# Kernel tuning notes

Measured on AMD Instinct MI355X. Metric: run time of the kernel, lower is better.

## Reference

```python
import jax, jax.numpy as jnp
import numpy as np

V = 1000   # vocab_size
E = 1024   # encoder_output_dim
D = 512    # decoder_hidden_dim
A = 512    # attention_hidden_dim
T = 128    # token_embedding_size
B = 128    # batch
P = 196    # num_pix (14x14)
L = 257    # latex length -> 256 decode steps


def setup_inputs() -> dict:
    key = jax.random.key(0)
    ks = jax.random.split(key, 16)
    def p(k, shape, scale=0.05):
        return (jax.random.normal(k, shape, jnp.float32) * scale)
    return dict(
        features=jax.random.normal(ks[0], (B, P, E), jnp.float32),
        latexes=jax.random.randint(ks[1], (B, L), 0, V),
        emb=p(ks[2], (V, T)),
        Wenc=p(ks[3], (A, E)), benc=jnp.zeros((A,), jnp.float32),
        Wdec=p(ks[4], (A, D)), bdec=jnp.zeros((A,), jnp.float32),
        Wattn=p(ks[5], (1, A)), battn=jnp.zeros((1,), jnp.float32),
        W1ih=p(ks[6], (4 * D, E + T)), W1hh=p(ks[7], (4 * D, D)),
        b1ih=jnp.zeros((4 * D,), jnp.float32), b1hh=jnp.zeros((4 * D,), jnp.float32),
        W2ih=p(ks[8], (4 * D, D)), W2hh=p(ks[9], (4 * D, D)),
        b2ih=jnp.zeros((4 * D,), jnp.float32), b2hh=jnp.zeros((4 * D,), jnp.float32),
        Wh0=p(ks[10], (D, E)), bh0=jnp.zeros((D,), jnp.float32),
        Wc0=p(ks[11], (D, E)), bc0=jnp.zeros((D,), jnp.float32),
        Wg=p(ks[12], (E, D)), bg=jnp.zeros((E,), jnp.float32),
        Wf=p(ks[13], (V, D)), bf=jnp.zeros((V,), jnp.float32),
    )


def _lstm_cell(x, h, c, Wih, Whh, bih, bhh):
    # torch.nn.LSTMCell: gates order i, f, g, o
    g = x @ Wih.T + bih + h @ Whh.T + bhh
    i, f, gg, o = jnp.split(g, 4, axis=1)
    c_new = jax.nn.sigmoid(f) * c + jax.nn.sigmoid(i) * jnp.tanh(gg)
    h_new = jax.nn.sigmoid(o) * jnp.tanh(c_new)
    return h_new, c_new


def reference(features, latexes, emb, Wenc, benc, Wdec, bdec, Wattn, battn,
              W1ih, W1hh, b1ih, b1hh, W2ih, W2hh, b2ih, b2hh,
              Wh0, bh0, Wc0, bc0, Wg, bg, Wf, bf):
    seq_length = latexes.shape[1] - 1
    embeds = emb[latexes]                      # [B, L, T]
    mean_enc = features.mean(axis=1)           # [B, E]
    h1 = mean_enc @ Wh0.T + bh0
    c1 = mean_enc @ Wc0.T + bc0
    h2, c2 = h1, c1
    # encoder branch of attention is step-invariant; hoist out of the loop
    enc_t = features @ Wenc.T + benc           # [B, P, A]
    wa = Wattn[0]                              # [A]
    ba = battn[0]

    def step(carry, emb_s):
        h1, c1, h2, c2 = carry
        dec_t = h2 @ Wdec.T + bdec                         # [B, A]
        attn = jnp.tanh(enc_t + dec_t[:, None, :]) @ wa + ba  # [B, P]
        alpha = jax.nn.softmax(attn, axis=1)
        awe = jnp.einsum('bp,bpe->be', alpha, features)    # [B, E]
        x1 = jnp.concatenate([emb_s, awe], axis=1)         # [B, T+E]
        # NOTE: original computes gate = sigmoid(Wg h2 + bg) and multiplies the
        # attention encoding AFTER lstm1_input was built -> dead code; omitted.
        h1n, c1n = _lstm_cell(x1, h1, c1, W1ih, W1hh, b1ih, b1hh)
        h2n, c2n = _lstm_cell(h1n, h2, c2, W2ih, W2hh, b2ih, b2hh)
        out = h2n @ Wf.T + bf                              # [B, V]
        return (h1n, c1n, h2n, c2n), (out, alpha)

    emb_seq = jnp.swapaxes(embeds[:, :seq_length], 0, 1)   # [S, B, T]
    _, (preds, alphas) = jax.lax.scan(step, (h1, c1, h2, c2), emb_seq)
    preds = jnp.swapaxes(preds, 0, 1)                      # [B, S, V]
    alphas = jnp.swapaxes(alphas, 0, 1)                    # [B, S, P]
    return preds, alphas
```

## Files before the change

kernel.cpp:

```cpp
#include <hip/hip_runtime.h>
#include <hip/hip_bf16.h>
#include <stdint.h>

#define VV 1000
#define EE 1024
#define DD 512
#define AA 512
#define TT 128
#define BB 128
#define PP 196
#define SS 256

typedef unsigned short ushort_t;
typedef __attribute__((ext_vector_type(8))) short short8;
typedef __attribute__((ext_vector_type(4))) float floatx4;
typedef __attribute__((ext_vector_type(4))) unsigned short ushort4_t;
typedef __attribute__((ext_vector_type(8))) unsigned short ushort8_t;

__device__ __forceinline__ float bf2f(unsigned short h) {
    return __uint_as_float(((unsigned int)h) << 16);
}
__device__ __forceinline__ unsigned short f2bf(float x) {
    unsigned int u = __float_as_uint(x);
    unsigned int r = (u + 0x7fffu + ((u >> 16) & 1u)) >> 16;
    return (unsigned short)r;
}
__device__ __forceinline__ float sigmoidf_(float x) { return 1.f / (1.f + __expf(-x)); }
__device__ __forceinline__ float tanhf_(float x) {
    float e = __expf(2.f * x);
    return 1.f - 2.f / (e + 1.f);
}


__global__ void cvt_kernel(const float* __restrict__ src, ushort_t* __restrict__ dst, int n) {
    int i = blockIdx.x * 256 + threadIdx.x;
    if (i < n) dst[i] = f2bf(src[i]);
}

__global__ void mean_kernel(const float* __restrict__ feat, float* __restrict__ meanv) {
    int idx = blockIdx.x * 256 + threadIdx.x;
    int b = idx >> 10;
    int e = idx & 1023;
    const float* p = feat + (size_t)b * PP * 1024 + e;
    float s = 0.f;
    for (int pp = 0; pp < PP; ++pp) s += p[(size_t)pp * 1024];
    meanv[idx] = s * (1.f / 196.f);
}

__global__ __launch_bounds__(256) void init_kernel(
    const float* __restrict__ meanv, const float* __restrict__ Wh0, const float* __restrict__ bh0,
    const float* __restrict__ Wc0, const float* __restrict__ bc0,
    float* __restrict__ c1, float* __restrict__ c2,
    ushort_t* __restrict__ h1b, ushort_t* __restrict__ h2b) {
    int b = blockIdx.x, t = threadIdx.x;
    __shared__ float ml[1024];
    for (int i = t; i < 1024; i += 256) ml[i] = meanv[b * 1024 + i];
    __syncthreads();
    for (int d = t; d < 512; d += 256) {
        const float4* wh = (const float4*)(Wh0 + (size_t)d * 1024);
        const float4* wc = (const float4*)(Wc0 + (size_t)d * 1024);
        float ah = bh0[d], ac = bc0[d];
        #pragma unroll 4
        for (int j = 0; j < 256; ++j) {
            float4 w = wh[j];
            ah += w.x * ml[4 * j] + w.y * ml[4 * j + 1] + w.z * ml[4 * j + 2] + w.w * ml[4 * j + 3];
        }
        #pragma unroll 4
        for (int j = 0; j < 256; ++j) {
            float4 w = wc[j];
            ac += w.x * ml[4 * j] + w.y * ml[4 * j + 1] + w.z * ml[4 * j + 2] + w.w * ml[4 * j + 3];
        }
        c1[b * 512 + d] = ac;
        c2[b * 512 + d] = ac;
        ushort_t hb = f2bf(ah);
        h1b[b * 512 + d] = hb;
        h2b[b * 512 + d] = hb;
    }
}

__global__ __launch_bounds__(256) void enc_gemm(
    const ushort_t* __restrict__ feat_bf, const ushort_t* __restrict__ wenc_bf,
    const float* __restrict__ benc, ushort_t* __restrict__ enc_bf) {
    const int t = threadIdx.x, blk = blockIdx.x;
    const int bm = (blk % 392) * 64, bn = (blk / 392) * 64;
    const int lane = t & 63, wv = t >> 6;
    const int n = lane & 15, q = lane >> 4;
    const int arow = bm + wv * 16 + n;
    const short8* ap = (const short8*)(feat_bf + (size_t)arow * 1024 + q * 8);
    const short8* bp0 = (const short8*)(wenc_bf + (size_t)(bn + 0 * 16 + n) * 1024 + q * 8);
    const short8* bp1 = (const short8*)(wenc_bf + (size_t)(bn + 1 * 16 + n) * 1024 + q * 8);
    const short8* bp2 = (const short8*)(wenc_bf + (size_t)(bn + 2 * 16 + n) * 1024 + q * 8);
    const short8* bp3 = (const short8*)(wenc_bf + (size_t)(bn + 3 * 16 + n) * 1024 + q * 8);
    floatx4 acc0 = {0.f, 0.f, 0.f, 0.f}, acc1 = acc0, acc2 = acc0, acc3 = acc0;
    for (int ks = 0; ks < 32; ++ks) {
        short8 a8 = ap[ks * 4];
        acc0 = __builtin_amdgcn_mfma_f32_16x16x32_bf16(a8, bp0[ks * 4], acc0, 0, 0, 0);
        acc1 = __builtin_amdgcn_mfma_f32_16x16x32_bf16(a8, bp1[ks * 4], acc1, 0, 0, 0);
        acc2 = __builtin_amdgcn_mfma_f32_16x16x32_bf16(a8, bp2[ks * 4], acc2, 0, 0, 0);
        acc3 = __builtin_amdgcn_mfma_f32_16x16x32_bf16(a8, bp3[ks * 4], acc3, 0, 0, 0);
    }
    #pragma unroll
    for (int r = 0; r < 4; ++r) {
        int m = bm + wv * 16 + q * 4 + r;
        int a0 = bn + n;
        enc_bf[(size_t)m * 512 + a0] = f2bf(acc0[r] + benc[a0]);
        enc_bf[(size_t)m * 512 + a0 + 16] = f2bf(acc1[r] + benc[a0 + 16]);
        enc_bf[(size_t)m * 512 + a0 + 32] = f2bf(acc2[r] + benc[a0 + 32]);
        enc_bf[(size_t)m * 512 + a0 + 48] = f2bf(acc3[r] + benc[a0 + 48]);
    }
}


__global__ __launch_bounds__(256) void step_attn_preds(
    const ushort_t* __restrict__ enc_bf, const ushort_t* __restrict__ feat_bf,
    const ushort_t* __restrict__ wdec_bf, const ushort_t* __restrict__ wf_bf,
    const ushort_t* __restrict__ emb_bf, ushort_t* __restrict__ x1_bf,
    const ushort_t* __restrict__ h2cur, const int* __restrict__ latexes,
    const float* __restrict__ wattn, const float* __restrict__ battn,
    const float* __restrict__ bdec, const float* __restrict__ bfv,
    float* __restrict__ out, int s) {
    const int t = threadIdx.x;
    const int blk = blockIdx.x;
    if (blk < BB) {
        if (s >= SS) return;
        const int b = blk;
        __shared__ float dec_lds[512];
        __shared__ float wa_lds[512];
        __shared__ float h2row[512];
        __shared__ float red[256];
        __shared__ float attn_lds[256];
        __shared__ float alpha_lds[200];
        for (int i = t; i < 512; i += 256) {
            h2row[i] = bf2f(h2cur[b * 512 + i]);
            wa_lds[i] = wattn[i];
        }
        __syncthreads();
        for (int d = t; d < 512; d += 256) {
            const ushort8_t* wr = (const ushort8_t*)(wdec_bf + (size_t)d * 512);
            float acc = 0.f;
            #pragma unroll 4
            for (int j = 0; j < 64; ++j) {
                ushort8_t w8 = wr[j];
                const float* h8 = &h2row[j * 8];
                #pragma unroll
                for (int u = 0; u < 8; ++u) acc += bf2f(w8[u]) * h8[u];
            }
            dec_lds[d] = acc + bdec[d];
        }
        __syncthreads();
        const int wv = t >> 6, lane = t & 63;
        for (int p = wv; p < PP; p += 4) {
            const ushort8_t ev = *(const ushort8_t*)(enc_bf + ((size_t)(b * PP + p)) * 512 + lane * 8);
            float acc = 0.f;
            #pragma unroll
            for (int u = 0; u < 8; ++u) {
                float x = bf2f(ev[u]) + dec_lds[lane * 8 + u];
                acc += wa_lds[lane * 8 + u] * tanhf_(x);
            }
            #pragma unroll
            for (int off = 32; off > 0; off >>= 1) acc += __shfl_xor(acc, off, 64);
            if (lane == 0) attn_lds[p] = acc + battn[0];
        }
        __syncthreads();
        float logit = (t < PP) ? attn_lds[t] : -1e30f;
        red[t] = logit;
        __syncthreads();
        for (int st = 128; st > 0; st >>= 1) {
            if (t < st) red[t] = fmaxf(red[t], red[t + st]);
            __syncthreads();
        }
        float mx = red[0];
        __syncthreads();
        float e = (t < PP) ? __expf(logit - mx) : 0.f;
        red[t] = e;
        __syncthreads();
        for (int st = 128; st > 0; st >>= 1) {
            if (t < st) red[t] += red[t + st];
            __syncthreads();
        }
        float inv = 1.f / red[0];
        float a = e * inv;
        if (t < PP) {
            alpha_lds[t] = a;
            out[(size_t)32768000 + (size_t)b * 50176 + (size_t)s * 196 + t] = a;
        }
        __syncthreads();
        float a0 = 0.f, a1 = 0.f, a2 = 0.f, a3 = 0.f;
        const int e0 = t * 4;
        for (int p = 0; p < PP; ++p) {
            float av = alpha_lds[p];
            ushort4_t f4 = *(const ushort4_t*)(feat_bf + ((size_t)(b * PP + p)) * 1024 + e0);
            a0 += av * bf2f(f4[0]);
            a1 += av * bf2f(f4[1]);
            a2 += av * bf2f(f4[2]);
            a3 += av * bf2f(f4[3]);
        }
        ushort4_t o4;
        o4[0] = f2bf(a0); o4[1] = f2bf(a1); o4[2] = f2bf(a2); o4[3] = f2bf(a3);
        *(ushort4_t*)(x1_bf + (size_t)b * 1152 + 128 + e0) = o4;
        if (t < TT) {
            int tok = latexes[b * 257 + s];
            x1_bf[(size_t)b * 1152 + t] = emb_bf[tok * TT + t];
        }
    } else {
        if (s == 0) return;
        const int wg2 = blk - BB;
        const int v0 = wg2 * 16;
        const int lane = t & 63, wv = t >> 6;
        const int n = lane & 15, q = lane >> 4;
        const int vrow = v0 + n;
        const int vclamp = vrow < VV ? vrow : VV - 1;
        const short8* bp = (const short8*)(wf_bf + (size_t)vclamp * 512 + q * 8);
        const int m0 = 2 * wv * 16 + n;
        const short8* ap0 = (const short8*)(h2cur + (size_t)m0 * 512 + q * 8);
        const short8* ap1 = (const short8*)(h2cur + (size_t)(m0 + 16) * 512 + q * 8);
        floatx4 acc0 = {0.f, 0.f, 0.f, 0.f}, acc1 = acc0;
        for (int ks = 0; ks < 16; ++ks) {
            short8 b8 = bp[ks * 4];
            acc0 = __builtin_amdgcn_mfma_f32_16x16x32_bf16(ap0[ks * 4], b8, acc0, 0, 0, 0);
            acc1 = __builtin_amdgcn_mfma_f32_16x16x32_bf16(ap1[ks * 4], b8, acc1, 0, 0, 0);
        }
        if (vrow < VV) {
            float cb = bfv[vrow];
            size_t so = (size_t)(s - 1) * 1000 + vrow;
            #pragma unroll
            for (int r = 0; r < 4; ++r) {
                int br = 2 * wv * 16 + q * 4 + r;
                out[(size_t)br * 256000 + so] = acc0[r] + cb;
                out[(size_t)(br + 16) * 256000 + so] = acc1[r] + cb;
            }
        }
    }
}

__global__ __launch_bounds__(256) void lstm_cell_kernel(
    const ushort_t* __restrict__ A1, int k1, const ushort_t* __restrict__ Wih,
    const ushort_t* __restrict__ A2, const ushort_t* __restrict__ Whh,
    const float* __restrict__ bih, const float* __restrict__ bhh,
    float* __restrict__ cst, ushort_t* __restrict__ hout) {
    const int t = threadIdx.x, wg = blockIdx.x;
    const int d0 = wg * 4;
    const int lane = t & 63, wv = t >> 6;
    const int n = lane & 15, q = lane >> 4;
    const int col = (n >> 2) * 512 + d0 + (n & 3);
    const int m0 = 2 * wv * 16 + n;
    floatx4 acc0 = {0.f, 0.f, 0.f, 0.f}, acc1 = acc0;
    {
        const short8* bp = (const short8*)(Wih + (size_t)col * k1 + q * 8);
        const short8* a0 = (const short8*)(A1 + (size_t)m0 * k1 + q * 8);
        const short8* a1 = (const short8*)(A1 + (size_t)(m0 + 16) * k1 + q * 8);
        const int nk = k1 >> 5;
        for (int ks = 0; ks < nk; ++ks) {
            short8 b8 = bp[ks * 4];
            acc0 = __builtin_amdgcn_mfma_f32_16x16x32_bf16(a0[ks * 4], b8, acc0, 0, 0, 0);
            acc1 = __builtin_amdgcn_mfma_f32_16x16x32_bf16(a1[ks * 4], b8, acc1, 0, 0, 0);
        }
    }
    {
        const short8* bp = (const short8*)(Whh + (size_t)col * 512 + q * 8);
        const short8* a0 = (const short8*)(A2 + (size_t)m0 * 512 + q * 8);
        const short8* a1 = (const short8*)(A2 + (size_t)(m0 + 16) * 512 + q * 8);
        for (int ks = 0; ks < 16; ++ks) {
            short8 b8 = bp[ks * 4];
            acc0 = __builtin_amdgcn_mfma_f32_16x16x32_bf16(a0[ks * 4], b8, acc0, 0, 0, 0);
            acc1 = __builtin_amdgcn_mfma_f32_16x16x32_bf16(a1[ks * 4], b8, acc1, 0, 0, 0);
        }
    }
    __shared__ float glds[128][16];
    #pragma unroll
    for (int r = 0; r < 4; ++r) {
        glds[2 * wv * 16 + q * 4 + r][n] = acc0[r];
        glds[2 * wv * 16 + 16 + q * 4 + r][n] = acc1[r];
    }
    __syncthreads();
    for (int idx = t; idx < 512; idx += 256) {
        int bb = idx >> 2, dj = idx & 3;
        int d = d0 + dj;
        float gi = glds[bb][dj] + bih[d] + bhh[d];
        float gf = glds[bb][4 + dj] + bih[512 + d] + bhh[512 + d];
        float gg = glds[bb][8 + dj] + bih[1024 + d] + bhh[1024 + d];
        float go = glds[bb][12 + dj] + bih[1536 + d] + bhh[1536 + d];
        float co = cst[bb * 512 + d];
        float cn = sigmoidf_(gf) * co + sigmoidf_(gi) * tanhf_(gg);
        float hn = sigmoidf_(go) * tanhf_(cn);
        cst[bb * 512 + d] = cn;
        hout[bb * 512 + d] = f2bf(hn);
    }
}

extern "C" void kernel_launch(void* const* d_in, const int* in_sizes, int n_in,
                              void* d_out, int out_size, void* d_ws, size_t ws_size,
                              hipStream_t stream) {
    const float* features = (const float*)d_in[0];
    const int* latexes = (const int*)d_in[1];
    const float* emb = (const float*)d_in[2];
    const float* Wenc = (const float*)d_in[3];
    const float* benc = (const float*)d_in[4];
    const float* Wdec = (const float*)d_in[5];
    const float* bdec = (const float*)d_in[6];
    const float* Wattn = (const float*)d_in[7];
    const float* battn = (const float*)d_in[8];
    const float* W1ih = (const float*)d_in[9];
    const float* W1hh = (const float*)d_in[10];
    const float* b1ih = (const float*)d_in[11];
    const float* b1hh = (const float*)d_in[12];
    const float* W2ih = (const float*)d_in[13];
    const float* W2hh = (const float*)d_in[14];
    const float* b2ih = (const float*)d_in[15];
    const float* b2hh = (const float*)d_in[16];
    const float* Wh0 = (const float*)d_in[17];
    const float* bh0 = (const float*)d_in[18];
    const float* Wc0 = (const float*)d_in[19];
    const float* bc0 = (const float*)d_in[20];
    const float* Wf = (const float*)d_in[23];
    const float* bfv = (const float*)d_in[24];
    float* out = (float*)d_out;

    char* ws = (char*)d_ws;
    size_t off = 0;
    auto alloc = [&](size_t bytes) {
        void* p = ws + off;
        off += (bytes + 255) & ~(size_t)255;
        return p;
    };
    ushort_t* feat_bf = (ushort_t*)alloc(25690112ull * 2);
    ushort_t* enc_bf = (ushort_t*)alloc(12845056ull * 2);
    ushort_t* w1ih_bf = (ushort_t*)alloc(2359296ull * 2);
    ushort_t* w1hh_bf = (ushort_t*)alloc(1048576ull * 2);
    ushort_t* w2ih_bf = (ushort_t*)alloc(1048576ull * 2);
    ushort_t* w2hh_bf = (ushort_t*)alloc(1048576ull * 2);
    ushort_t* wf_bf = (ushort_t*)alloc(512000ull * 2);
    ushort_t* wdec_bf = (ushort_t*)alloc(262144ull * 2);
    ushort_t* wenc_bf = (ushort_t*)alloc(524288ull * 2);
    ushort_t* emb_bf = (ushort_t*)alloc(128000ull * 2);
    float* meanv = (float*)alloc(131072ull * 4);
    float* c1 = (float*)alloc(65536ull * 4);
    float* c2 = (float*)alloc(65536ull * 4);
    ushort_t* h1b0 = (ushort_t*)alloc(65536ull * 2);
    ushort_t* h1b1 = (ushort_t*)alloc(65536ull * 2);
    ushort_t* h2b0 = (ushort_t*)alloc(65536ull * 2);
    ushort_t* h2b1 = (ushort_t*)alloc(65536ull * 2);
    ushort_t* x1_bf = (ushort_t*)alloc(147456ull * 2);
    ushort_t* h1b[2] = {h1b0, h1b1};
    ushort_t* h2b[2] = {h2b0, h2b1};

    auto cv = [&](const float* s, ushort_t* d, int n) {
        cvt_kernel<<<(n + 255) / 256, 256, 0, stream>>>(s, d, n);
    };
    cv(features, feat_bf, 25690112);
    cv(Wenc, wenc_bf, 524288);
    cv(W1ih, w1ih_bf, 2359296);
    cv(W1hh, w1hh_bf, 1048576);
    cv(W2ih, w2ih_bf, 1048576);
    cv(W2hh, w2hh_bf, 1048576);
    cv(Wf, wf_bf, 512000);
    cv(Wdec, wdec_bf, 262144);
    cv(emb, emb_bf, 128000);
    mean_kernel<<<512, 256, 0, stream>>>(features, meanv);
    init_kernel<<<128, 256, 0, stream>>>(meanv, Wh0, bh0, Wc0, bc0, c1, c2, h1b[0], h2b[0]);
    enc_gemm<<<3136, 256, 0, stream>>>(feat_bf, wenc_bf, benc, enc_bf);

    for (int s = 0; s <= SS; ++s) {
        int cur = s & 1, nxt = 1 - cur;
        step_attn_preds<<<191, 256, 0, stream>>>(enc_bf, feat_bf, wdec_bf, wf_bf, emb_bf, x1_bf,
                                                 h2b[cur], latexes, Wattn, battn, bdec, bfv, out, s);
        if (s < SS) {
            lstm_cell_kernel<<<128, 256, 0, stream>>>(x1_bf, 1152, w1ih_bf, h1b[cur], w1hh_bf,
                                                      b1ih, b1hh, c1, h1b[nxt]);
            lstm_cell_kernel<<<128, 256, 0, stream>>>(h1b[nxt], 512, w2ih_bf, h2b[cur], w2hh_bf,
                                                      b2ih, b2hh, c2, h2b[nxt]);
        }
    }
}
```

Baseline: 27.86 ms.

## Fuse decode loop into one persistent kernel with software grid barriers

Replaces the per-step launches of the attention/preds kernel and two LSTM cell kernels with a single persistent kernel of 256 blocks. Steps are separated by atomic flag-based grid barriers, and LSTM cell state and biases stay in registers across steps. Sigmoid and tanh now use exp2 plus a hardware reciprocal. The goal is to remove roughly 770 kernel launch and drain overheads, at the cost of spin-wait barrier latency and the risk of deadlock if all 256 blocks are not co-resident.

```diff
diff --git a/kernel.cpp b/kernel.cpp
--- a/kernel.cpp
+++ b/kernel.cpp
@@ -22,19 +22,24 @@
 }
 __device__ __forceinline__ unsigned short f2bf(float x) {
     unsigned int u = __float_as_uint(x);
-    unsigned int r = (u + 0x7fffu + ((u >> 16) & 1u)) >> 16;
-    return (unsigned short)r;
-}
-__device__ __forceinline__ float sigmoidf_(float x) { return 1.f / (1.f + __expf(-x)); }
-__device__ __forceinline__ float tanhf_(float x) {
-    float e = __expf(2.f * x);
-    return 1.f - 2.f / (e + 1.f);
+    return (unsigned short)((u + 0x7fffu + ((u >> 16) & 1u)) >> 16);
+}
+#define LOG2E 1.4426950408889634f
+__device__ __forceinline__ float fsig(float x) {
+    return __builtin_amdgcn_rcpf(1.f + exp2f(-LOG2E * x));
+}
+__device__ __forceinline__ float ftanh(float x) {
+    return 1.f - 2.f * __builtin_amdgcn_rcpf(1.f + exp2f(2.f * LOG2E * x));
 }
 
 
 __global__ void cvt_kernel(const float* __restrict__ src, ushort_t* __restrict__ dst, int n) {
     int i = blockIdx.x * 256 + threadIdx.x;
     if (i < n) dst[i] = f2bf(src[i]);
+}
+
+__global__ void zero_bar(int* __restrict__ p) {
+    p[blockIdx.x * 256 + threadIdx.x] = 0;
 }
 
 __global__ void mean_kernel(const float* __restrict__ feat, float* __restrict__ meanv) {
@@ -111,138 +116,52 @@
 }
 
 
-__global__ __launch_bounds__(256) void step_attn_preds(
-    const ushort_t* __restrict__ enc_bf, const ushort_t* __restrict__ feat_bf,
-    const ushort_t* __restrict__ wdec_bf, const ushort_t* __restrict__ wf_bf,
-    const ushort_t* __restrict__ emb_bf, ushort_t* __restrict__ x1_bf,
-    const ushort_t* __restrict__ h2cur, const int* __restrict__ latexes,
-    const float* __restrict__ wattn, const float* __restrict__ battn,
-    const float* __restrict__ bdec, const float* __restrict__ bfv,
-    float* __restrict__ out, int s) {
-    const int t = threadIdx.x;
-    const int blk = blockIdx.x;
-    if (blk < BB) {
-        if (s >= SS) return;
-        const int b = blk;
-        __shared__ float dec_lds[512];
-        __shared__ float wa_lds[512];
-        __shared__ float h2row[512];
-        __shared__ float red[256];
-        __shared__ float attn_lds[256];
-        __shared__ float alpha_lds[200];
-        for (int i = t; i < 512; i += 256) {
-            h2row[i] = bf2f(h2cur[b * 512 + i]);
-            wa_lds[i] = wattn[i];
+struct SmA {
+    float dec[512];
+    float wa[512];
+    float h2r[512];
+    float red[256];
+    float attn[256];
+    float alpha[200];
+};
+union SmU {
+    SmA a;
+    float glds[128][17];
+};
+
+__device__ __forceinline__ void gridbar(int* flags, int* go, int gen) {
+    __syncthreads();
+    if (blockIdx.x == 0) {
+        const int t = threadIdx.x;
+        if (t > 0) {
+            while (__hip_atomic_load(&flags[t], __ATOMIC_RELAXED, __HIP_MEMORY_SCOPE_AGENT) < gen)
+                __builtin_amdgcn_s_sleep(1);
         }
         __syncthreads();
-        for (int d = t; d < 512; d += 256) {
-            const ushort8_t* wr = (const ushort8_t*)(wdec_bf + (size_t)d * 512);
-            float acc = 0.f;
-            #pragma unroll 4
-            for (int j = 0; j < 64; ++j) {
-                ushort8_t w8 = wr[j];
-                const float* h8 = &h2row[j * 8];
-                #pragma unroll
-                for (int u = 0; u < 8; ++u) acc += bf2f(w8[u]) * h8[u];
-            }
-            dec_lds[d] = acc + bdec[d];
+        if (t == 0) {
+            __builtin_amdgcn_fence(__ATOMIC_SEQ_CST, "agent");
+            __hip_atomic_store(go, gen, __ATOMIC_RELAXED, __HIP_MEMORY_SCOPE_AGENT);
+        }
+    } else {
+        if (threadIdx.x == 0) {
+            __builtin_amdgcn_fence(__ATOMIC_SEQ_CST, "agent");
+            __hip_atomic_store(&flags[blockIdx.x], gen, __ATOMIC_RELAXED, __HIP_MEMORY_SCOPE_AGENT);
+            while (__hip_atomic_load(go, __ATOMIC_RELAXED, __HIP_MEMORY_SCOPE_AGENT) < gen)
+                __builtin_amdgcn_s_sleep(1);
         }
         __syncthreads();
-        const int wv = t >> 6, lane = t & 63;
-        for (int p = wv; p < PP; p += 4) {
-            const ushort8_t ev = *(const ushort8_t*)(enc_bf + ((size_t)(b * PP + p)) * 512 + lane * 8);
-            float acc = 0.f;
-            #pragma unroll
-            for (int u = 0; u < 8; ++u) {
-                float x = bf2f(ev[u]) + dec_lds[lane * 8 + u];
-                acc += wa_lds[lane * 8 + u] * tanhf_(x);
-            }
-            #pragma unroll
-            for (int off = 32; off > 0; off >>= 1) acc += __shfl_xor(acc, off, 64);
-            if (lane == 0) attn_lds[p] = acc + battn[0];
-        }
-        __syncthreads();
-        float logit = (t < PP) ? attn_lds[t] : -1e30f;
-        red[t] = logit;
-        __syncthreads();
-        for (int st = 128; st > 0; st >>= 1) {
-            if (t < st) red[t] = fmaxf(red[t], red[t + st]);
-            __syncthreads();
-        }
-        float mx = red[0];
-        __syncthreads();
-        float e = (t < PP) ? __expf(logit - mx) : 0.f;
-        red[t] = e;
-        __syncthreads();
-        for (int st = 128; st > 0; st >>= 1) {
-            if (t < st) red[t] += red[t + st];
-            __syncthreads();
-        }
-        float inv = 1.f / red[0];
-        float a = e * inv;
-        if (t < PP) {
-            alpha_lds[t] = a;
-            out[(size_t)32768000 + (size_t)b * 50176 + (size_t)s * 196 + t] = a;
-        }
-        __syncthreads();
-        float a0 = 0.f, a1 = 0.f, a2 = 0.f, a3 = 0.f;
-        const int e0 = t * 4;
-        for (int p = 0; p < PP; ++p) {
-            float av = alpha_lds[p];
-            ushort4_t f4 = *(const ushort4_t*)(feat_bf + ((size_t)(b * PP + p)) * 1024 + e0);
-            a0 += av * bf2f(f4[0]);
-            a1 += av * bf2f(f4[1]);
-            a2 += av * bf2f(f4[2]);
-            a3 += av * bf2f(f4[3]);
-        }
-        ushort4_t o4;
-        o4[0] = f2bf(a0); o4[1] = f2bf(a1); o4[2] = f2bf(a2); o4[3] = f2bf(a3);
-        *(ushort4_t*)(x1_bf + (size_t)b * 1152 + 128 + e0) = o4;
-        if (t < TT) {
-            int tok = latexes[b * 257 + s];
-            x1_bf[(size_t)b * 1152 + t] = emb_bf[tok * TT + t];
-        }
-    } else {
-        if (s == 0) return;
-        const int wg2 = blk - BB;
-        const int v0 = wg2 * 16;
-        const int lane = t & 63, wv = t >> 6;
-        const int n = lane & 15, q = lane >> 4;
-        const int vrow = v0 + n;
-        const int vclamp = vrow < VV ? vrow : VV - 1;
-        const short8* bp = (const short8*)(wf_bf + (size_t)vclamp * 512 + q * 8);
-        const int m0 = 2 * wv * 16 + n;
-        const short8* ap0 = (const short8*)(h2cur + (size_t)m0 * 512 + q * 8);
-        const short8* ap1 = (const short8*)(h2cur + (size_t)(m0 + 16) * 512 + q * 8);
-        floatx4 acc0 = {0.f, 0.f, 0.f, 0.f}, acc1 = acc0;
-        for (int ks = 0; ks < 16; ++ks) {
-            short8 b8 = bp[ks * 4];
-            acc0 = __builtin_amdgcn_mfma_f32_16x16x32_bf16(ap0[ks * 4], b8, acc0, 0, 0, 0);
-            acc1 = __builtin_amdgcn_mfma_f32_16x16x32_bf16(ap1[ks * 4], b8, acc1, 0, 0, 0);
-        }
-        if (vrow < VV) {
-            float cb = bfv[vrow];
-            size_t so = (size_t)(s - 1) * 1000 + vrow;
-            #pragma unroll
-            for (int r = 0; r < 4; ++r) {
-                int br = 2 * wv * 16 + q * 4 + r;
-                out[(size_t)br * 256000 + so] = acc0[r] + cb;
-                out[(size_t)(br + 16) * 256000 + so] = acc1[r] + cb;
-            }
-        }
-    }
-}
-
-__global__ __launch_bounds__(256) void lstm_cell_kernel(
-    const ushort_t* __restrict__ A1, int k1, const ushort_t* __restrict__ Wih,
+    }
+    __builtin_amdgcn_fence(__ATOMIC_ACQUIRE, "agent");
+}
+
+__device__ __forceinline__ void lstm_phase(
+    const ushort_t* __restrict__ A1, const int k1, const ushort_t* __restrict__ Wih,
     const ushort_t* __restrict__ A2, const ushort_t* __restrict__ Whh,
-    const float* __restrict__ bih, const float* __restrict__ bhh,
-    float* __restrict__ cst, ushort_t* __restrict__ hout) {
-    const int t = threadIdx.x, wg = blockIdx.x;
-    const int d0 = wg * 4;
+    const float* bs, float* creg, ushort_t* __restrict__ hout,
+    const int wg, const int t, float (*glds)[17]) {
     const int lane = t & 63, wv = t >> 6;
     const int n = lane & 15, q = lane >> 4;
-    const int col = (n >> 2) * 512 + d0 + (n & 3);
+    const int col = (n >> 2) * 512 + wg * 4 + (n & 3);
     const int m0 = 2 * wv * 16 + n;
     floatx4 acc0 = {0.f, 0.f, 0.f, 0.f}, acc1 = acc0;
     {
@@ -266,25 +185,196 @@
             acc1 = __builtin_amdgcn_mfma_f32_16x16x32_bf16(a1[ks * 4], b8, acc1, 0, 0, 0);
         }
     }
-    __shared__ float glds[128][16];
     #pragma unroll
     for (int r = 0; r < 4; ++r) {
         glds[2 * wv * 16 + q * 4 + r][n] = acc0[r];
         glds[2 * wv * 16 + 16 + q * 4 + r][n] = acc1[r];
     }
     __syncthreads();
-    for (int idx = t; idx < 512; idx += 256) {
-        int bb = idx >> 2, dj = idx & 3;
-        int d = d0 + dj;
-        float gi = glds[bb][dj] + bih[d] + bhh[d];
-        float gf = glds[bb][4 + dj] + bih[512 + d] + bhh[512 + d];
-        float gg = glds[bb][8 + dj] + bih[1024 + d] + bhh[1024 + d];
-        float go = glds[bb][12 + dj] + bih[1536 + d] + bhh[1536 + d];
-        float co = cst[bb * 512 + d];
-        float cn = sigmoidf_(gf) * co + sigmoidf_(gi) * tanhf_(gg);
-        float hn = sigmoidf_(go) * tanhf_(cn);
-        cst[bb * 512 + d] = cn;
-        hout[bb * 512 + d] = f2bf(hn);
+    const int dj = t & 3, d = wg * 4 + dj;
+    #pragma unroll
+    for (int k = 0; k < 2; ++k) {
+        const int bb = (t >> 2) + 64 * k;
+        float gi = glds[bb][dj] + bs[0];
+        float gf = glds[bb][4 + dj] + bs[1];
+        float gg = glds[bb][8 + dj] + bs[2];
+        float go = glds[bb][12 + dj] + bs[3];
+        float cn = fsig(gf) * creg[k] + fsig(gi) * ftanh(gg);
+        creg[k] = cn;
+        hout[bb * 512 + d] = f2bf(fsig(go) * ftanh(cn));
+    }
+}
+
+__global__ __launch_bounds__(256) void fused_loop(
+    const ushort_t* __restrict__ enc_bf, const ushort_t* __restrict__ feat_bf,
+    const ushort_t* __restrict__ wdec_bf, const ushort_t* __restrict__ wf_bf,
+    const ushort_t* __restrict__ emb_bf,
+    const ushort_t* __restrict__ w1ih, const ushort_t* __restrict__ w1hh,
+    const ushort_t* __restrict__ w2ih, const ushort_t* __restrict__ w2hh,
+    const int* __restrict__ latexes,
+    const float* __restrict__ wattn, const float* __restrict__ battn,
+    const float* __restrict__ bdec, const float* __restrict__ bfv,
+    const float* __restrict__ b1ih, const float* __restrict__ b1hh,
+    const float* __restrict__ b2ih, const float* __restrict__ b2hh,
+    const float* __restrict__ c1g, const float* __restrict__ c2g,
+    ushort_t* __restrict__ h1b0, ushort_t* __restrict__ h1b1,
+    ushort_t* __restrict__ h2b0, ushort_t* __restrict__ h2b1,
+    ushort_t* __restrict__ x1_bf,
+    int* __restrict__ flags, int* __restrict__ go,
+    float* __restrict__ out) {
+    const int t = threadIdx.x, blk = blockIdx.x;
+    __shared__ SmU sm;
+
+    float c1r[2], c2r[2], bs1[4], bs2[4];
+    const int dj = t & 3;
+    if (blk < BB) {
+        const int d = blk * 4 + dj;
+        #pragma unroll
+        for (int g = 0; g < 4; ++g) {
+            bs1[g] = b1ih[g * 512 + d] + b1hh[g * 512 + d];
+            bs2[g] = b2ih[g * 512 + d] + b2hh[g * 512 + d];
+        }
+        c1r[0] = c1g[(t >> 2) * 512 + d];
+        c1r[1] = c1g[((t >> 2) + 64) * 512 + d];
+        c2r[0] = c2g[(t >> 2) * 512 + d];
+        c2r[1] = c2g[((t >> 2) + 64) * 512 + d];
+    }
+    const float ba = battn[0];
+    int gen = 0;
+
+    for (int s = 0; s <= SS; ++s) {
+        const int cur = s & 1;
+        const ushort_t* h1c = cur ? h1b1 : h1b0;
+        ushort_t* h1n = cur ? h1b0 : h1b1;
+        const ushort_t* h2c = cur ? h2b1 : h2b0;
+        ushort_t* h2n = cur ? h2b0 : h2b1;
+
+        if (blk < BB) {
+            if (s < SS) {
+                const int b = blk;
+                for (int i = t; i < 512; i += 256) {
+                    sm.a.h2r[i] = bf2f(h2c[b * 512 + i]);
+                    sm.a.wa[i] = wattn[i];
+                }
+                __syncthreads();
+                {
+                    float a0 = 0.f, a1 = 0.f;
+                    const ushort8_t* w0 = (const ushort8_t*)(wdec_bf + (size_t)t * 512);
+                    const ushort8_t* w1 = (const ushort8_t*)(wdec_bf + (size_t)(t + 256) * 512);
+                    for (int j = 0; j < 64; ++j) {
+                        ushort8_t x0 = w0[j], x1v = w1[j];
+                        const float* h8 = &sm.a.h2r[j * 8];
+                        #pragma unroll
+                        for (int u = 0; u < 8; ++u) {
+                            a0 += bf2f(x0[u]) * h8[u];
+                            a1 += bf2f(x1v[u]) * h8[u];
+                        }
+                    }
+                    sm.a.dec[t] = a0 + bdec[t];
+                    sm.a.dec[t + 256] = a1 + bdec[t + 256];
+                }
+                __syncthreads();
+                const int wv = t >> 6, lane = t & 63;
+                float dec8[8], wa8[8];
+                #pragma unroll
+                for (int u = 0; u < 8; ++u) {
+                    dec8[u] = sm.a.dec[lane * 8 + u];
+                    wa8[u] = sm.a.wa[lane * 8 + u];
+                }
+                for (int p = wv; p < PP; p += 4) {
+                    const ushort8_t ev =
+                        *(const ushort8_t*)(enc_bf + ((size_t)(b * PP + p)) * 512 + lane * 8);
+                    float acc = 0.f;
+                    #pragma unroll
+                    for (int u = 0; u < 8; ++u) {
+                        float x = bf2f(ev[u]) + dec8[u];
+                        float r = __builtin_amdgcn_rcpf(1.f + exp2f(2.f * LOG2E * x));
+                        acc += wa8[u] * (1.f - 2.f * r);
+                    }
+                    #pragma unroll
+                    for (int off = 32; off > 0; off >>= 1) acc += __shfl_xor(acc, off, 64);
+                    if (lane == 0) sm.a.attn[p] = acc + ba;
+                }
+                __syncthreads();
+                float logit = (t < PP) ? sm.a.attn[t] : -1e30f;
+                sm.a.red[t] = logit;
+                __syncthreads();
+                for (int st = 128; st > 0; st >>= 1) {
+                    if (t < st) sm.a.red[t] = fmaxf(sm.a.red[t], sm.a.red[t + st]);
+                    __syncthreads();
+                }
+                float mx = sm.a.red[0];
+                __syncthreads();
+                float e = (t < PP) ? exp2f((logit - mx) * LOG2E) : 0.f;
+                sm.a.red[t] = e;
+                __syncthreads();
+                for (int st = 128; st > 0; st >>= 1) {
+                    if (t < st) sm.a.red[t] += sm.a.red[t + st];
+                    __syncthreads();
+                }
+                float a = e * __builtin_amdgcn_rcpf(sm.a.red[0]);
+                if (t < PP) {
+                    sm.a.alpha[t] = a;
+                    out[(size_t)32768000 + (size_t)b * 50176 + (size_t)s * 196 + t] = a;
+                }
+                __syncthreads();
+                float a0 = 0.f, a1 = 0.f, a2 = 0.f, a3 = 0.f;
+                const int e0 = t * 4;
+                for (int p = 0; p < PP; ++p) {
+                    float av = sm.a.alpha[p];
+                    ushort4_t f4 = *(const ushort4_t*)(feat_bf + ((size_t)(b * PP + p)) * 1024 + e0);
+                    a0 += av * bf2f(f4[0]);
+                    a1 += av * bf2f(f4[1]);
+                    a2 += av * bf2f(f4[2]);
+                    a3 += av * bf2f(f4[3]);
+                }
+                ushort4_t o4;
+                o4[0] = f2bf(a0); o4[1] = f2bf(a1); o4[2] = f2bf(a2); o4[3] = f2bf(a3);
+                *(ushort4_t*)(x1_bf + (size_t)b * 1152 + 128 + e0) = o4;
+                if (t < TT) {
+                    int tok = latexes[b * 257 + s];
+                    x1_bf[(size_t)b * 1152 + t] = emb_bf[tok * TT + t];
+                }
+            }
+        } else if (blk < 191) {
+            if (s > 0) {
+                const int v0 = (blk - BB) * 16;
+                const int lane = t & 63, wv = t >> 6;
+                const int n = lane & 15, q = lane >> 4;
+                const int vrow = v0 + n;
+                const int vclamp = vrow < VV ? vrow : VV - 1;
+                const short8* bp = (const short8*)(wf_bf + (size_t)vclamp * 512 + q * 8);
+                const int m0 = 2 * wv * 16 + n;
+                const short8* ap0 = (const short8*)(h2c + (size_t)m0 * 512 + q * 8);
+                const short8* ap1 = (const short8*)(h2c + (size_t)(m0 + 16) * 512 + q * 8);
+                floatx4 acc0 = {0.f, 0.f, 0.f, 0.f}, acc1 = acc0;
+                for (int ks = 0; ks < 16; ++ks) {
+                    short8 b8 = bp[ks * 4];
+                    acc0 = __builtin_amdgcn_mfma_f32_16x16x32_bf16(ap0[ks * 4], b8, acc0, 0, 0, 0);
+                    acc1 = __builtin_amdgcn_mfma_f32_16x16x32_bf16(ap1[ks * 4], b8, acc1, 0, 0, 0);
+                }
+                if (vrow < VV) {
+                    float cb = bfv[vrow];
+                    size_t so = (size_t)(s - 1) * 1000 + vrow;
+                    #pragma unroll
+                    for (int r = 0; r < 4; ++r) {
+                        int br = 2 * wv * 16 + q * 4 + r;
+                        out[(size_t)br * 256000 + so] = acc0[r] + cb;
+                        out[(size_t)(br + 16) * 256000 + so] = acc1[r] + cb;
+                    }
+                }
+            }
+        }
+        if (s == SS) break;
+        gridbar(flags, go, ++gen);
+
+        if (blk < BB)
+            lstm_phase(x1_bf, 1152, w1ih, h1c, w1hh, bs1, c1r, h1n, blk, t, sm.glds);
+        gridbar(flags, go, ++gen);
+
+        if (blk < BB)
+            lstm_phase(h1n, 512, w2ih, h2c, w2hh, bs2, c2r, h2n, blk, t, sm.glds);
+        gridbar(flags, go, ++gen);
     }
 }
 
@@ -341,8 +431,7 @@
     ushort_t* h2b0 = (ushort_t*)alloc(65536ull * 2);
     ushort_t* h2b1 = (ushort_t*)alloc(65536ull * 2);
     ushort_t* x1_bf = (ushort_t*)alloc(147456ull * 2);
-    ushort_t* h1b[2] = {h1b0, h1b1};
-    ushort_t* h2b[2] = {h2b0, h2b1};
+    int* barmem = (int*)alloc(512 * 4);
 
     auto cv = [&](const float* s, ushort_t* d, int n) {
         cvt_kernel<<<(n + 255) / 256, 256, 0, stream>>>(s, d, n);
@@ -356,19 +445,13 @@
     cv(Wf, wf_bf, 512000);
     cv(Wdec, wdec_bf, 262144);
     cv(emb, emb_bf, 128000);
+    zero_bar<<<2, 256, 0, stream>>>(barmem);
     mean_kernel<<<512, 256, 0, stream>>>(features, meanv);
-    init_kernel<<<128, 256, 0, stream>>>(meanv, Wh0, bh0, Wc0, bc0, c1, c2, h1b[0], h2b[0]);
+    init_kernel<<<128, 256, 0, stream>>>(meanv, Wh0, bh0, Wc0, bc0, c1, c2, h1b0, h2b0);
     enc_gemm<<<3136, 256, 0, stream>>>(feat_bf, wenc_bf, benc, enc_bf);
 
-    for (int s = 0; s <= SS; ++s) {
-        int cur = s & 1, nxt = 1 - cur;
-        step_attn_preds<<<191, 256, 0, stream>>>(enc_bf, feat_bf, wdec_bf, wf_bf, emb_bf, x1_bf,
-                                                 h2b[cur], latexes, Wattn, battn, bdec, bfv, out, s);
-        if (s < SS) {
-            lstm_cell_kernel<<<128, 256, 0, stream>>>(x1_bf, 1152, w1ih_bf, h1b[cur], w1hh_bf,
-                                                      b1ih, b1hh, c1, h1b[nxt]);
-            lstm_cell_kernel<<<128, 256, 0, stream>>>(h1b[nxt], 512, w2ih_bf, h2b[cur], w2hh_bf,
-                                                      b2ih, b2hh, c2, h2b[nxt]);
-        }
-    }
-}
+    fused_loop<<<256, 256, 0, stream>>>(
+        enc_bf, feat_bf, wdec_bf, wf_bf, emb_bf, w1ih_bf, w1hh_bf, w2ih_bf, w2hh_bf,
+        latexes, Wattn, battn, bdec, bfv, b1ih, b1hh, b2ih, b2hh, c1, c2,
+        h1b0, h1b1, h2b0, h2b1, x1_bf, barmem, barmem + 256, out);
+}
```

Result: slower. 37.56 ms (+34.8%).
